# Optimization experiments

Hardware: AMD Instinct MI355X
Metric: run time of the kernel (lower is better)

Reference implementation:

```python
import jax, jax.numpy as jnp
import numpy as np

NEG_SLOPE = 0.01  # torch F.leaky_relu default
N_USER = 100000
N_ITEM = 100000
N_EDGE = 640000
D = 128
N_LAYERS = 3  # 1 input + num_hidden_layers(1) + 1 output layer


def setup_inputs() -> dict:
    key = jax.random.key(0)
    ks = jax.random.split(key, 10)
    scale = 1.0 / np.sqrt(D)
    return {
        "h_user": jax.random.normal(ks[0], (N_USER, D), dtype=jnp.float32),
        "h_item": jax.random.normal(ks[1], (N_ITEM, D), dtype=jnp.float32),
        # W[layer, etype] : etype 0 = user-follows->user, 1 = user-clicks->item, 2 = item-clicked_by->user
        "W": jax.random.normal(ks[2], (N_LAYERS, 3, D, D), dtype=jnp.float32) * scale,
        "b": jnp.zeros((N_LAYERS, 3, D), dtype=jnp.float32),
        "follows_src": jax.random.randint(ks[3], (N_EDGE,), 0, N_USER, dtype=jnp.int32),
        "follows_dst": jax.random.randint(ks[4], (N_EDGE,), 0, N_USER, dtype=jnp.int32),
        "clicks_src": jax.random.randint(ks[5], (N_EDGE,), 0, N_USER, dtype=jnp.int32),
        "clicks_dst": jax.random.randint(ks[6], (N_EDGE,), 0, N_ITEM, dtype=jnp.int32),
        "cb_src": jax.random.randint(ks[7], (N_EDGE,), 0, N_ITEM, dtype=jnp.int32),
        "cb_dst": jax.random.randint(ks[8], (N_EDGE,), 0, N_USER, dtype=jnp.int32),
    }


def _etype_conv(h_src, W, b, src, dst, n_dst):
    """Per-etype Linear on src nodes, copy_u gather, mean-aggregate at dst."""
    Wh = h_src @ W + b                     # [N_src, D] dense transform (once per node)
    msg = Wh[src]                          # [E, D] gather
    s = jax.ops.segment_sum(msg, dst, num_segments=n_dst)
    cnt = jax.ops.segment_sum(jnp.ones((src.shape[0],), dtype=Wh.dtype), dst, num_segments=n_dst)
    return s / jnp.maximum(cnt, 1.0)[:, None]  # mean; isolated nodes -> 0


def _rgcn_forward(h_user, h_item, W, b, follows_src, follows_dst,
                  clicks_src, clicks_dst, cb_src, cb_dst):
    hu, hi = h_user, h_item
    for l in range(N_LAYERS):
        # per-etype mean aggregation, then cross-etype 'sum' (DGL multi_update_all)
        agg_u = (_etype_conv(hu, W[l, 0], b[l, 0], follows_src, follows_dst, N_USER)
                 + _etype_conv(hi, W[l, 2], b[l, 2], cb_src, cb_dst, N_USER))
        agg_i = _etype_conv(hu, W[l, 1], b[l, 1], clicks_src, clicks_dst, N_ITEM)
        hu = jax.nn.leaky_relu(agg_u, NEG_SLOPE)
        hi = jax.nn.leaky_relu(agg_i, NEG_SLOPE)
    return jnp.stack([hu, hi])  # [2, 100000, 128]


def reference(h_user, h_item, W, b, follows_src, follows_dst,
              clicks_src, clicks_dst, cb_src, cb_dst):
    return _rgcn_forward(h_user, h_item, W, b, follows_src, follows_dst,
                         clicks_src, clicks_dst, cb_src, cb_dst)
```

## Files before the change

kernel.cpp:

```cpp
#include <hip/hip_runtime.h>

typedef unsigned short u16;
typedef _Float16 f16;
typedef __attribute__((ext_vector_type(2))) _Float16 f16x2;
typedef __attribute__((ext_vector_type(8))) _Float16 f16x8;
typedef __attribute__((ext_vector_type(2))) float f32x2;
typedef __attribute__((ext_vector_type(4))) float f32x4;

#define D 128

__global__ __launch_bounds__(256) void k_convert(const float* __restrict__ in,
                                                 u16* __restrict__ out, int n8) {
  int i = blockIdx.x * 256 + threadIdx.x;
  if (i >= n8) return;
  const float4* ip = (const float4*)in;
  float4 a = ip[i * 2], b = ip[i * 2 + 1];
  f16x8 v = {(f16)a.x, (f16)a.y, (f16)a.z, (f16)a.w,
             (f16)b.x, (f16)b.y, (f16)b.z, (f16)b.w};
  *(f16x8*)(out + (size_t)i * 8) = v;
}

__global__ __launch_bounds__(256) void k_convW(const float* __restrict__ W,
                                               u16* __restrict__ Wt, int total) {
  int idx = blockIdx.x * 256 + threadIdx.x;
  if (idx >= total) return;
  int mat = idx >> 14;
  int k = (idx >> 7) & 127;
  int n = idx & 127;
  f16 v = (f16)W[idx];
  ((f16*)Wt)[(size_t)mat * 16384 + n * 128 + k] = v;
}

__global__ __launch_bounds__(256) void k_count(const int* __restrict__ dst,
                                               int* __restrict__ cnt, int nE) {
  int e = blockIdx.x * 256 + threadIdx.x;
  if (e < nE) atomicAdd(&cnt[dst[e]], 1);
}

__global__ __launch_bounds__(256) void k_scanA(const int* __restrict__ cnt,
                                               int* __restrict__ part, int n) {
  int t = threadIdx.x;
  int idx = blockIdx.x * 1024 + t * 4;
  int4 v = {0, 0, 0, 0};
  if (idx + 3 < n)
    v = *(const int4*)(cnt + idx);
  else {
    if (idx < n) v.x = cnt[idx];
    if (idx + 1 < n) v.y = cnt[idx + 1];
    if (idx + 2 < n) v.z = cnt[idx + 2];
    if (idx + 3 < n) v.w = cnt[idx + 3];
  }
  int s = v.x + v.y + v.z + v.w;
  for (int off = 1; off < 64; off <<= 1) s += __shfl_down(s, off, 64);
  __shared__ int ws[4];
  if ((t & 63) == 0) ws[t >> 6] = s;
  __syncthreads();
  if (t == 0) part[blockIdx.x] = ws[0] + ws[1] + ws[2] + ws[3];
}

__global__ __launch_bounds__(1024) void k_scanB(int* __restrict__ part, int n_part) {
  __shared__ int sh[1024];
  int t = threadIdx.x;
  int v = (t < n_part) ? part[t] : 0;
  sh[t] = v;
  __syncthreads();
  for (int off = 1; off < 1024; off <<= 1) {
    int u = (t >= off) ? sh[t - off] : 0;
    __syncthreads();
    sh[t] += u;
    __syncthreads();
  }
  if (t < n_part) part[t] = sh[t] - v;
}

__global__ __launch_bounds__(256) void k_scanC(const int* __restrict__ cnt,
                                               const int* __restrict__ part,
                                               int* __restrict__ rs,
                                               int n, int total) {
  int t = threadIdx.x;
  int idx = blockIdx.x * 1024 + t * 4;
  int4 v = {0, 0, 0, 0};
  if (idx + 3 < n)
    v = *(const int4*)(cnt + idx);
  else {
    if (idx < n) v.x = cnt[idx];
    if (idx + 1 < n) v.y = cnt[idx + 1];
    if (idx + 2 < n) v.z = cnt[idx + 2];
    if (idx + 3 < n) v.w = cnt[idx + 3];
  }
  int s = v.x + v.y + v.z + v.w;
  int inc = s;
  int lane = t & 63, w = t >> 6;
  for (int off = 1; off < 64; off <<= 1) {
    int u = __shfl_up(inc, off, 64);
    if (lane >= off) inc += u;
  }
  __shared__ int ws[4];
  if (lane == 63) ws[w] = inc;
  __syncthreads();
  int woff = 0;
  for (int i = 0; i < w; ++i) woff += ws[i];
  int ex = part[blockIdx.x] + woff + inc - s;
  int4 r;
  r.x = ex;
  r.y = ex + v.x;
  r.z = r.y + v.y;
  r.w = r.z + v.z;
  if (idx + 3 < n)
    *(int4*)(rs + idx) = r;
  else {
    if (idx < n) rs[idx] = r.x;
    if (idx + 1 < n) rs[idx + 1] = r.y;
    if (idx + 2 < n) rs[idx + 2] = r.z;
    if (idx + 3 < n) rs[idx + 3] = r.w;
  }
  if (blockIdx.x == 0 && t == 0) rs[n] = total;
}

__global__ __launch_bounds__(256) void k_fill(const int* __restrict__ src,
                                              const int* __restrict__ dst,
                                              const int* __restrict__ rs,
                                              int* __restrict__ cnt,
                                              int* __restrict__ csr, int nE, int soff) {
  int e = blockIdx.x * 256 + threadIdx.x;
  if (e < nE) {
    int d = dst[e];
    int p = atomicSub(&cnt[d], 1);
    csr[rs[d] + p - 1] = src[e] + soff;
  }
}

__global__ __launch_bounds__(256) void k_agg3(
    const u16* __restrict__ h_all, const int* __restrict__ csr,
    const int* __restrict__ rs, u16* __restrict__ M_all, int N3) {
  int wave = (blockIdx.x * 256 + threadIdx.x) >> 6;
  int lane = threadIdx.x & 63;
  int l16 = lane & 15;
  int w = wave * 4 + (lane >> 4);
  bool valid = w < N3;
  int wc = valid ? w : 0;
  int e = rs[wc];
  int en = valid ? rs[wc + 1] : 0;
  int deg = en - e;
  f32x2 ac0 = {0.f, 0.f}, ac1 = {0.f, 0.f}, ac2 = {0.f, 0.f}, ac3 = {0.f, 0.f};
  const char* hb = (const char*)h_all;
  unsigned loff = (unsigned)l16 * 16u;

  while (__any(e < en)) {
    bool a0 = e < en, a1 = e + 1 < en;
    int s0 = 0, s1 = 0;
    if (a0) s0 = csr[e];
    if (a1) s1 = csr[e + 1];
    f16x8 v0 = {0, 0, 0, 0, 0, 0, 0, 0}, v1 = {0, 0, 0, 0, 0, 0, 0, 0};
    if (a0) v0 = *(const f16x8*)(hb + ((unsigned)s0 * 256u + loff));
    if (a1) v1 = *(const f16x8*)(hb + ((unsigned)s1 * 256u + loff));
    ac0 += (f32x2){(float)v0[0], (float)v0[1]};
    ac1 += (f32x2){(float)v0[2], (float)v0[3]};
    ac2 += (f32x2){(float)v0[4], (float)v0[5]};
    ac3 += (f32x2){(float)v0[6], (float)v0[7]};
    ac0 += (f32x2){(float)v1[0], (float)v1[1]};
    ac1 += (f32x2){(float)v1[2], (float)v1[3]};
    ac2 += (f32x2){(float)v1[4], (float)v1[5]};
    ac3 += (f32x2){(float)v1[6], (float)v1[7]};
    e += 2;
  }

  if (valid) {
    float inv = deg ? 1.0f / (float)deg : 0.f;
    f16x8 r = {(f16)(ac0[0] * inv), (f16)(ac0[1] * inv),
               (f16)(ac1[0] * inv), (f16)(ac1[1] * inv),
               (f16)(ac2[0] * inv), (f16)(ac2[1] * inv),
               (f16)(ac3[0] * inv), (f16)(ac3[1] * inv)};
    *(f16x8*)((char*)M_all + ((unsigned)wc * 256u + loff)) = r;
  }
}

template <int NE, int OUTF32>
__device__ __forceinline__ void gemm_body(
    f16 (*Wt)[128][136],
    const u16* __restrict__ mA, const u16* __restrict__ mBp,
    const u16* __restrict__ wtA, const u16* __restrict__ wtB,
    const float* __restrict__ bA, const float* __restrict__ bB,
    const int* __restrict__ rsA, const int* __restrict__ rsB,
    u16* __restrict__ o16, float* __restrict__ o32, int M, int blk) {
  int tid = threadIdx.x;
  {
    const f16x8* wa = (const f16x8*)wtA;
    for (int idx = tid; idx < 128 * 16; idx += 256) {
      int n = idx >> 4, c = idx & 15;
      *(f16x8*)&Wt[0][n][c * 8] = wa[idx];
    }
    if (NE == 2) {
      const f16x8* wb = (const f16x8*)wtB;
      for (int idx = tid; idx < 128 * 16; idx += 256) {
        int n = idx >> 4, c = idx & 15;
        *(f16x8*)&Wt[1][n][c * 8] = wb[idx];
      }
    }
  }
  __syncthreads();

  int lane = tid & 63, w = tid >> 6;
  int lr = lane & 15;
  int lk = (lane >> 4) * 8;
  long row0 = (long)blk * 128 + w * 32;

  f32x4 acc[2][8];
#pragma unroll
  for (int rt = 0; rt < 2; rt++)
#pragma unroll
    for (int n = 0; n < 8; n++) acc[rt][n] = (f32x4){0.f, 0.f, 0.f, 0.f};

#pragma unroll
  for (int e = 0; e < NE; ++e) {
    const f16* mm = (const f16*)((e == 0) ? mA : mBp);
#pragma unroll
    for (int ks = 0; ks < 4; ++ks) {
      int k0 = ks * 32 + lk;
      f16x8 bf[8];
#pragma unroll
      for (int n = 0; n < 8; n++) bf[n] = *(const f16x8*)&Wt[e][n * 16 + lr][k0];
#pragma unroll
      for (int rt = 0; rt < 2; rt++) {
        long r = row0 + rt * 16 + lr;
        if (r >= M) r = M - 1;
        f16x8 af = *(const f16x8*)(mm + r * D + k0);
#pragma unroll
        for (int n = 0; n < 8; n++)
          acc[rt][n] = __builtin_amdgcn_mfma_f32_16x16x32_f16(af, bf[n], acc[rt][n], 0, 0, 0);
      }
    }
  }

  float bAr[8], bBr[8];
#pragma unroll
  for (int n = 0; n < 8; n++) {
    bAr[n] = bA[n * 16 + lr];
    bBr[n] = (NE == 2) ? bB[n * 16 + lr] : 0.f;
  }

#pragma unroll
  for (int rt = 0; rt < 2; rt++) {
    long rbase = row0 + rt * 16 + (lane >> 4) * 4;
#pragma unroll
    for (int i = 0; i < 4; i++) {
      long r = rbase + i;
      if (r < M) {
        bool mAok = rsA[r + 1] > rsA[r];
        bool mBok = (NE == 2) && (rsB[r + 1] > rsB[r]);
#pragma unroll
        for (int n = 0; n < 8; n++) {
          int col = n * 16 + lr;
          float v = acc[rt][n][i];
          if (mAok) v += bAr[n];
          if (mBok) v += bBr[n];
          v = v > 0.f ? v : 0.01f * v;
          if (OUTF32)
            o32[r * D + col] = v;
          else
            ((f16*)o16)[r * D + col] = (f16)v;
        }
      }
    }
  }
}

template <int OUTF32>
__global__ __launch_bounds__(256) void k_gemm2(
    const u16* __restrict__ M_all, const u16* __restrict__ Wl,
    const float* __restrict__ bl, const int* __restrict__ rs_all,
    u16* __restrict__ h_all, float* __restrict__ out,
    int NU, int NI, int nbI) {
  __shared__ __align__(16) f16 Wt[2][128][136];
  if ((int)blockIdx.x < nbI) {
    gemm_body<1, OUTF32>(Wt,
                         M_all + (size_t)NU * D, nullptr,
                         Wl + 16384, nullptr,
                         bl + D, nullptr,
                         rs_all + NU, nullptr,
                         h_all + (size_t)NU * D, out + (size_t)NU * D, NI,
                         blockIdx.x);
  } else {
    gemm_body<2, OUTF32>(Wt,
                         M_all, M_all + (size_t)(NU + NI) * D,
                         Wl, Wl + 2 * 16384,
                         bl, bl + 2 * D,
                         rs_all, rs_all + NU + NI,
                         h_all, out, NU, blockIdx.x - nbI);
  }
}

extern "C" void kernel_launch(void* const* d_in, const int* in_sizes, int n_in,
                              void* d_out, int out_size, void* d_ws, size_t ws_size,
                              hipStream_t stream) {
  const float* h_user = (const float*)d_in[0];
  const float* h_item = (const float*)d_in[1];
  const float* W = (const float*)d_in[2];
  const float* bb = (const float*)d_in[3];
  const int* f_src = (const int*)d_in[4];
  const int* f_dst = (const int*)d_in[5];
  const int* c_src = (const int*)d_in[6];
  const int* c_dst = (const int*)d_in[7];
  const int* cb_src = (const int*)d_in[8];
  const int* cb_dst = (const int*)d_in[9];

  const int NU = in_sizes[0] / D;
  const int NI = in_sizes[1] / D;
  const int nEf = in_sizes[4], nEc = in_sizes[6], nEcb = in_sizes[8];
  const int N3 = NU + NI + NU;
  const int nE = nEf + nEc + nEcb;

  char* p = (char*)d_ws;
  auto alloc = [&](size_t bytes) {
    char* r = p;
    p += (bytes + 255) & ~(size_t)255;
    return r;
  };
  int* cnt_all = (int*)alloc((size_t)N3 * 4);
  int* rs_all = (int*)alloc((size_t)(N3 + 1) * 4);
  int* part = (int*)alloc(1024 * 4);
  u16* Wtg = (u16*)alloc((size_t)9 * 16384 * 2);
  int* csr_all = (int*)alloc((size_t)nE * 4);
  u16* h_all = (u16*)alloc((size_t)(NU + NI) * D * 2);
  u16* M_all = (u16*)alloc((size_t)N3 * D * 2);
  (void)ws_size;

  hipMemsetAsync(cnt_all, 0, (size_t)N3 * 4, stream);

  k_convert<<<(NU * D / 8 + 255) / 256, 256, 0, stream>>>(h_user, h_all, NU * D / 8);
  k_convert<<<(NI * D / 8 + 255) / 256, 256, 0, stream>>>(h_item, h_all + (size_t)NU * D,
                                                          NI * D / 8);
  k_convW<<<(9 * 16384 + 255) / 256, 256, 0, stream>>>(W, Wtg, 9 * 16384);

  k_count<<<(nEf + 255) / 256, 256, 0, stream>>>(f_dst, cnt_all, nEf);
  k_count<<<(nEc + 255) / 256, 256, 0, stream>>>(c_dst, cnt_all + NU, nEc);
  k_count<<<(nEcb + 255) / 256, 256, 0, stream>>>(cb_dst, cnt_all + NU + NI, nEcb);

  int n_part = (N3 + 1023) / 1024;
  k_scanA<<<n_part, 256, 0, stream>>>(cnt_all, part, N3);
  k_scanB<<<1, 1024, 0, stream>>>(part, n_part);
  k_scanC<<<n_part, 256, 0, stream>>>(cnt_all, part, rs_all, N3, nE);

  k_fill<<<(nEf + 255) / 256, 256, 0, stream>>>(f_src, f_dst, rs_all, cnt_all,
                                                csr_all, nEf, 0);
  k_fill<<<(nEc + 255) / 256, 256, 0, stream>>>(c_src, c_dst, rs_all + NU, cnt_all + NU,
                                                csr_all, nEc, 0);
  k_fill<<<(nEcb + 255) / 256, 256, 0, stream>>>(cb_src, cb_dst, rs_all + NU + NI,
                                                 cnt_all + NU + NI, csr_all, nEcb, NU);

  int nbI = (NI + 127) / 128;
  int nbU = (NU + 127) / 128;
  int agg_blocks = ((N3 + 3) / 4 + 3) / 4;

  for (int l = 0; l < 3; ++l) {
    const u16* Wl = Wtg + (size_t)l * 3 * 16384;
    const float* bl = bb + (size_t)l * 3 * D;

    k_agg3<<<agg_blocks, 256, 0, stream>>>(h_all, csr_all, rs_all, M_all, N3);

    if (l < 2)
      k_gemm2<0><<<nbI + nbU, 256, 0, stream>>>(M_all, Wl, bl, rs_all, h_all,
                                                (float*)d_out, NU, NI, nbI);
    else
      k_gemm2<1><<<nbI + nbU, 256, 0, stream>>>(M_all, Wl, bl, rs_all, h_all,
                                                (float*)d_out, NU, NI, nbI);
  }
}
```

Measured before the change: 586.6 us.

## Merge per-etype count/fill launches, accumulate in fp16, read weights from global

Collapses the three count kernels and three fill kernels into single launches covering all edge types, which cuts launch overhead. The aggregation kernel now accumulates in packed fp16 instead of fp32 and unrolls four edges per iteration, aiming for more memory-level parallelism and cheaper arithmetic. The GEMM drops its shared-memory staging of weights and reads them directly from global/L2, removing LDS use and a barrier. The fp16 accumulation costs precision for high-degree nodes, and direct global weight reads may add memory traffic.

```diff
diff --git a/kernel.cpp b/kernel.cpp
--- a/kernel.cpp
+++ b/kernel.cpp
@@ -2,9 +2,7 @@
 
 typedef unsigned short u16;
 typedef _Float16 f16;
-typedef __attribute__((ext_vector_type(2))) _Float16 f16x2;
 typedef __attribute__((ext_vector_type(8))) _Float16 f16x8;
-typedef __attribute__((ext_vector_type(2))) float f32x2;
 typedef __attribute__((ext_vector_type(4))) float f32x4;
 
 #define D 128
@@ -31,10 +29,17 @@
   ((f16*)Wt)[(size_t)mat * 16384 + n * 128 + k] = v;
 }
 
-__global__ __launch_bounds__(256) void k_count(const int* __restrict__ dst,
-                                               int* __restrict__ cnt, int nE) {
+__global__ __launch_bounds__(256) void k_count3(
+    const int* __restrict__ fd, const int* __restrict__ cd,
+    const int* __restrict__ cbd, int* __restrict__ cnt,
+    int NU, int NI, int nf, int nc, int ncb) {
   int e = blockIdx.x * 256 + threadIdx.x;
-  if (e < nE) atomicAdd(&cnt[dst[e]], 1);
+  if (e < nf)
+    atomicAdd(&cnt[fd[e]], 1);
+  else if (e < nf + nc)
+    atomicAdd(&cnt[NU + cd[e - nf]], 1);
+  else if (e < nf + nc + ncb)
+    atomicAdd(&cnt[NU + NI + cbd[e - nf - nc]], 1);
 }
 
 __global__ __launch_bounds__(256) void k_scanA(const int* __restrict__ cnt,
@@ -117,17 +122,27 @@
   if (blockIdx.x == 0 && t == 0) rs[n] = total;
 }
 
-__global__ __launch_bounds__(256) void k_fill(const int* __restrict__ src,
-                                              const int* __restrict__ dst,
-                                              const int* __restrict__ rs,
-                                              int* __restrict__ cnt,
-                                              int* __restrict__ csr, int nE, int soff) {
+__global__ __launch_bounds__(256) void k_fill3(
+    const int* __restrict__ fs, const int* __restrict__ fd,
+    const int* __restrict__ cs, const int* __restrict__ cd,
+    const int* __restrict__ cbs, const int* __restrict__ cbd,
+    const int* __restrict__ rs, int* __restrict__ cnt, int* __restrict__ csr,
+    int NU, int NI, int nf, int nc, int ncb) {
   int e = blockIdx.x * 256 + threadIdx.x;
-  if (e < nE) {
-    int d = dst[e];
-    int p = atomicSub(&cnt[d], 1);
-    csr[rs[d] + p - 1] = src[e] + soff;
-  }
+  int d, s;
+  if (e < nf) {
+    d = fd[e];
+    s = fs[e];
+  } else if (e < nf + nc) {
+    d = NU + cd[e - nf];
+    s = cs[e - nf];
+  } else if (e < nf + nc + ncb) {
+    d = NU + NI + cbd[e - nf - nc];
+    s = cbs[e - nf - nc] + NU;
+  } else
+    return;
+  int p = atomicSub(&cnt[d], 1);
+  csr[rs[d] + p - 1] = s;
 }
 
 __global__ __launch_bounds__(256) void k_agg3(
@@ -142,65 +157,47 @@
   int e = rs[wc];
   int en = valid ? rs[wc + 1] : 0;
   int deg = en - e;
-  f32x2 ac0 = {0.f, 0.f}, ac1 = {0.f, 0.f}, ac2 = {0.f, 0.f}, ac3 = {0.f, 0.f};
+  f16x8 acc0 = {0, 0, 0, 0, 0, 0, 0, 0};
+  f16x8 acc1 = {0, 0, 0, 0, 0, 0, 0, 0};
   const char* hb = (const char*)h_all;
   unsigned loff = (unsigned)l16 * 16u;
 
   while (__any(e < en)) {
-    bool a0 = e < en, a1 = e + 1 < en;
-    int s0 = 0, s1 = 0;
-    if (a0) s0 = csr[e];
-    if (a1) s1 = csr[e + 1];
+    bool a0 = e < en, a1 = e + 1 < en, a2 = e + 2 < en, a3 = e + 3 < en;
+    int s0 = a0 ? csr[e] : 0;
+    int s1 = a1 ? csr[e + 1] : 0;
+    int s2 = a2 ? csr[e + 2] : 0;
+    int s3 = a3 ? csr[e + 3] : 0;
     f16x8 v0 = {0, 0, 0, 0, 0, 0, 0, 0}, v1 = {0, 0, 0, 0, 0, 0, 0, 0};
+    f16x8 v2 = {0, 0, 0, 0, 0, 0, 0, 0}, v3 = {0, 0, 0, 0, 0, 0, 0, 0};
     if (a0) v0 = *(const f16x8*)(hb + ((unsigned)s0 * 256u + loff));
     if (a1) v1 = *(const f16x8*)(hb + ((unsigned)s1 * 256u + loff));
-    ac0 += (f32x2){(float)v0[0], (float)v0[1]};
-    ac1 += (f32x2){(float)v0[2], (float)v0[3]};
-    ac2 += (f32x2){(float)v0[4], (float)v0[5]};
-    ac3 += (f32x2){(float)v0[6], (float)v0[7]};
-    ac0 += (f32x2){(float)v1[0], (float)v1[1]};
-    ac1 += (f32x2){(float)v1[2], (float)v1[3]};
-    ac2 += (f32x2){(float)v1[4], (float)v1[5]};
-    ac3 += (f32x2){(float)v1[6], (float)v1[7]};
-    e += 2;
+    if (a2) v2 = *(const f16x8*)(hb + ((unsigned)s2 * 256u + loff));
+    if (a3) v3 = *(const f16x8*)(hb + ((unsigned)s3 * 256u + loff));
+    acc0 += v0;
+    acc1 += v1;
+    acc0 += v2;
+    acc1 += v3;
+    e += 4;
   }
 
   if (valid) {
-    float inv = deg ? 1.0f / (float)deg : 0.f;
-    f16x8 r = {(f16)(ac0[0] * inv), (f16)(ac0[1] * inv),
-               (f16)(ac1[0] * inv), (f16)(ac1[1] * inv),
-               (f16)(ac2[0] * inv), (f16)(ac2[1] * inv),
-               (f16)(ac3[0] * inv), (f16)(ac3[1] * inv)};
+    float invf = deg > 0 ? 1.0f / (float)deg : 0.f;
+    f16 hinv = (f16)invf;
+    f16x8 t = acc0 + acc1;
+    f16x8 r = t * hinv;
     *(f16x8*)((char*)M_all + ((unsigned)wc * 256u + loff)) = r;
   }
 }
 
 template <int NE, int OUTF32>
 __device__ __forceinline__ void gemm_body(
-    f16 (*Wt)[128][136],
     const u16* __restrict__ mA, const u16* __restrict__ mBp,
     const u16* __restrict__ wtA, const u16* __restrict__ wtB,
     const float* __restrict__ bA, const float* __restrict__ bB,
     const int* __restrict__ rsA, const int* __restrict__ rsB,
     u16* __restrict__ o16, float* __restrict__ o32, int M, int blk) {
-  int tid = threadIdx.x;
-  {
-    const f16x8* wa = (const f16x8*)wtA;
-    for (int idx = tid; idx < 128 * 16; idx += 256) {
-      int n = idx >> 4, c = idx & 15;
-      *(f16x8*)&Wt[0][n][c * 8] = wa[idx];
-    }
-    if (NE == 2) {
-      const f16x8* wb = (const f16x8*)wtB;
-      for (int idx = tid; idx < 128 * 16; idx += 256) {
-        int n = idx >> 4, c = idx & 15;
-        *(f16x8*)&Wt[1][n][c * 8] = wb[idx];
-      }
-    }
-  }
-  __syncthreads();
-
-  int lane = tid & 63, w = tid >> 6;
+  int tid = threadIdx.x, lane = tid & 63, w = tid >> 6;
   int lr = lane & 15;
   int lk = (lane >> 4) * 8;
   long row0 = (long)blk * 128 + w * 32;
@@ -214,12 +211,13 @@
 #pragma unroll
   for (int e = 0; e < NE; ++e) {
     const f16* mm = (const f16*)((e == 0) ? mA : mBp);
+    const f16* Wg = (const f16*)((e == 0) ? wtA : wtB);
 #pragma unroll
     for (int ks = 0; ks < 4; ++ks) {
       int k0 = ks * 32 + lk;
       f16x8 bf[8];
 #pragma unroll
-      for (int n = 0; n < 8; n++) bf[n] = *(const f16x8*)&Wt[e][n * 16 + lr][k0];
+      for (int n = 0; n < 8; n++) bf[n] = *(const f16x8*)(Wg + (n * 16 + lr) * D + k0);
 #pragma unroll
       for (int rt = 0; rt < 2; rt++) {
         long r = row0 + rt * 16 + lr;
@@ -271,18 +269,15 @@
     const float* __restrict__ bl, const int* __restrict__ rs_all,
     u16* __restrict__ h_all, float* __restrict__ out,
     int NU, int NI, int nbI) {
-  __shared__ __align__(16) f16 Wt[2][128][136];
   if ((int)blockIdx.x < nbI) {
-    gemm_body<1, OUTF32>(Wt,
-                         M_all + (size_t)NU * D, nullptr,
+    gemm_body<1, OUTF32>(M_all + (size_t)NU * D, nullptr,
                          Wl + 16384, nullptr,
                          bl + D, nullptr,
                          rs_all + NU, nullptr,
                          h_all + (size_t)NU * D, out + (size_t)NU * D, NI,
                          blockIdx.x);
   } else {
-    gemm_body<2, OUTF32>(Wt,
-                         M_all, M_all + (size_t)(NU + NI) * D,
+    gemm_body<2, OUTF32>(M_all, M_all + (size_t)(NU + NI) * D,
                          Wl, Wl + 2 * 16384,
                          bl, bl + 2 * D,
                          rs_all, rs_all + NU + NI,
@@ -332,21 +327,17 @@
                                                           NI * D / 8);
   k_convW<<<(9 * 16384 + 255) / 256, 256, 0, stream>>>(W, Wtg, 9 * 16384);
 
-  k_count<<<(nEf + 255) / 256, 256, 0, stream>>>(f_dst, cnt_all, nEf);
-  k_count<<<(nEc + 255) / 256, 256, 0, stream>>>(c_dst, cnt_all + NU, nEc);
-  k_count<<<(nEcb + 255) / 256, 256, 0, stream>>>(cb_dst, cnt_all + NU + NI, nEcb);
+  k_count3<<<(nE + 255) / 256, 256, 0, stream>>>(f_dst, c_dst, cb_dst, cnt_all,
+                                                 NU, NI, nEf, nEc, nEcb);
 
   int n_part = (N3 + 1023) / 1024;
   k_scanA<<<n_part, 256, 0, stream>>>(cnt_all, part, N3);
   k_scanB<<<1, 1024, 0, stream>>>(part, n_part);
   k_scanC<<<n_part, 256, 0, stream>>>(cnt_all, part, rs_all, N3, nE);
 
-  k_fill<<<(nEf + 255) / 256, 256, 0, stream>>>(f_src, f_dst, rs_all, cnt_all,
-                                                csr_all, nEf, 0);
-  k_fill<<<(nEc + 255) / 256, 256, 0, stream>>>(c_src, c_dst, rs_all + NU, cnt_all + NU,
-                                                csr_all, nEc, 0);
-  k_fill<<<(nEcb + 255) / 256, 256, 0, stream>>>(cb_src, cb_dst, rs_all + NU + NI,
-                                                 cnt_all + NU + NI, csr_all, nEcb, NU);
+  k_fill3<<<(nE + 255) / 256, 256, 0, stream>>>(f_src, f_dst, c_src, c_dst,
+                                                cb_src, cb_dst, rs_all, cnt_all,
+                                                csr_all, NU, NI, nEf, nEc, nEcb);
 
   int nbI = (NI + 127) / 128;
   int nbU = (NU + 127) / 128;
```

Result: slower. 625.5 us (+6.6%).
